# Kernel tuning notes

Measured on AMD Instinct MI355X. Metric: run time of the kernel, lower is better.

The kernel has to match this reference:

```python
import jax, jax.numpy as jnp
import numpy as np

B, T, H = 4096, 512, 512
GATE = 2 + H  # concat([x(1), h(H), mask(1)])


def setup_inputs() -> dict:
    key = jax.random.key(0)
    ks = jax.random.split(key, 20)
    s = 1.0 / np.sqrt(GATE)
    inp = {
        "x": jax.random.normal(ks[0], (B, T), jnp.float32),
        "x_last": jax.random.normal(ks[1], (B, T), jnp.float32),
        "interval": jax.random.uniform(ks[2], (B, T), jnp.float32),
        "mask": (jax.random.uniform(ks[3], (B, T)) > 0.3).astype(jnp.float32),
        # gamma decay layers
        "Wgx": jax.random.normal(ks[4], (1, 1), jnp.float32),
        "bgx": jnp.zeros((1,), jnp.float32),
        "Wgh": jax.random.normal(ks[5], (H, 1), jnp.float32),
        "bgh": jnp.zeros((H,), jnp.float32),
        # gate layers: Linear(GATE, H)
        "Wz": jax.random.normal(ks[6], (H, GATE), jnp.float32) * s,
        "bz": jnp.zeros((H,), jnp.float32),
        "Wr": jax.random.normal(ks[7], (H, GATE), jnp.float32) * s,
        "br": jnp.zeros((H,), jnp.float32),
        "Wh": jax.random.normal(ks[8], (H, GATE), jnp.float32) * s,
        "bh": jnp.zeros((H,), jnp.float32),
        # output head Linear(H, 1)
        "Wo": jax.random.normal(ks[9], (1, H), jnp.float32) / np.sqrt(H),
        "bo": jnp.zeros((1,), jnp.float32),
    }
    return inp


def reference(x, x_last, interval, mask, Wgx, bgx, Wgh, bgh,
              Wz, bz, Wr, br, Wh, bh, Wo, bo):
    # x, x_last, interval, mask: [B, T]; feature dim is 1 after unsqueeze
    x3 = x[..., None]            # [B, T, 1]
    xl3 = x_last[..., None]
    it3 = interval[..., None]
    m3 = mask[..., None]
    # mean(x*m, dim=1) * T / sum(m, dim=1) == sum(x*m)/sum(m)
    x_mean = jnp.sum(x3 * m3, axis=1) / jnp.sum(m3, axis=1)  # [B, 1]

    h0 = jnp.zeros((x.shape[0], Wz.shape[0]), x.dtype)
    # time-major stacks for scan: [T, B, 1]
    xs = (jnp.swapaxes(x3, 0, 1), jnp.swapaxes(xl3, 0, 1),
          jnp.swapaxes(m3, 0, 1), jnp.swapaxes(it3, 0, 1))

    def step(h, ts):
        xt, xl, mt, it = ts  # each [B, 1]
        gamma_x = jnp.exp(-jax.nn.relu(it @ Wgx.T + bgx))   # [B, 1]
        gamma_h = jnp.exp(-jax.nn.relu(it @ Wgh.T + bgh))   # [B, H]
        xi = mt * xt + (1.0 - mt) * (gamma_x * xl + (1.0 - gamma_x) * x_mean)
        h = gamma_h * h
        comb = jnp.concatenate([xi, h, mt], axis=1)          # [B, GATE]
        z = jax.nn.sigmoid(comb @ Wz.T + bz)
        r = jax.nn.sigmoid(comb @ Wr.T + br)
        comb_r = jnp.concatenate([xi, r * h, mt], axis=1)
        h_tilde = jnp.tanh(comb_r @ Wh.T + bh)
        h = (1.0 - z) * h + z * h_tilde
        return h, None

    h, _ = jax.lax.scan(step, h0, xs)
    return jax.nn.sigmoid(h @ Wo.T + bo)  # [B, 1]
```

## Files before the change

### kernel.cpp

```cpp
#include <hip/hip_runtime.h>
#include <stdint.h>

#define T_LEN 512
#define H_DIM 512
#define B_TOT 4096
#define GATE_D 514
#define CLUSTERS 16
#define RANKS 16
#define CROWS 256
#define OWNC 32
#define NTHR 512
#define BARPAD 256

typedef short s16x8 __attribute__((ext_vector_type(8)));
typedef float f32x4 __attribute__((ext_vector_type(4)));

__device__ __forceinline__ ushort f2bf(float f) {
    uint32_t u = __builtin_bit_cast(uint32_t, f);
    u += 0x7FFF + ((u >> 16) & 1);
    return (ushort)(u >> 16);
}
__device__ __forceinline__ float sigmoid_f(float x) {
    return 1.0f / (1.0f + __expf(-x));
}
__device__ __forceinline__ float tanh_f(float x) {
    float ax = fabsf(x);
    float e  = __expf(2.0f * ax);
    float t  = 1.0f - 2.0f / (e + 1.0f);
    return copysignf(t, x);
}
__device__ __forceinline__ void vm0() {
    asm volatile("s_waitcnt vmcnt(0)" ::: "memory");
}

__global__ void k_xmean(const float* __restrict__ x, const float* __restrict__ m,
                        float* __restrict__ xmean) {
    int b = blockIdx.x;
    int l = threadIdx.x;
    const float* xr = x + (size_t)b * T_LEN;
    const float* mr = m + (size_t)b * T_LEN;
    float sx = 0.f, sm = 0.f;
    #pragma unroll
    for (int i = 0; i < T_LEN / 64; ++i) {
        float mv = mr[l + i * 64];
        sx += xr[l + i * 64] * mv;
        sm += mv;
    }
    for (int off = 32; off; off >>= 1) {
        sx += __shfl_down(sx, off);
        sm += __shfl_down(sm, off);
    }
    if (l == 0) xmean[b] = sx / sm;
}

__global__ void k_init(unsigned int* barc) {
    int i = threadIdx.x + blockIdx.x * blockDim.x;
    if (i < CLUSTERS * BARPAD) barc[i] = 0u;
}

__device__ __forceinline__ void bar_slow(unsigned int* cnt, unsigned int target) {
    vm0();
    __syncthreads();
    if (threadIdx.x == 0) {
        __builtin_amdgcn_fence(__ATOMIC_RELEASE, "agent");
        __hip_atomic_fetch_add(cnt, 1u, __ATOMIC_RELAXED, __HIP_MEMORY_SCOPE_AGENT);
        while (__hip_atomic_load(cnt, __ATOMIC_RELAXED, __HIP_MEMORY_SCOPE_AGENT) < target)
            __builtin_amdgcn_s_sleep(1);
        __builtin_amdgcn_fence(__ATOMIC_ACQUIRE, "agent");
    }
    __syncthreads();
}

__device__ __forceinline__ void wave_arrive(unsigned int* cw, bool fastc) {
    vm0();
    if ((threadIdx.x & 63) == 0) {
        if (!fastc) __builtin_amdgcn_fence(__ATOMIC_RELEASE, "agent");
        __hip_atomic_fetch_add(cw, 1u, __ATOMIC_RELAXED, __HIP_MEMORY_SCOPE_AGENT);
    }
}
__device__ __forceinline__ void wave_wait(unsigned int* cw, unsigned int target, bool fastc) {
    while (__hip_atomic_load(cw, __ATOMIC_RELAXED, __HIP_MEMORY_SCOPE_AGENT) < target)
        __builtin_amdgcn_s_sleep(1);
    if (fastc) { asm volatile("buffer_inv" ::: "memory"); vm0(); }
    else __builtin_amdgcn_fence(__ATOMIC_ACQUIRE, "agent");
}

__global__ __launch_bounds__(NTHR) void k_grud(
    const float* __restrict__ x,   const float* __restrict__ xl,
    const float* __restrict__ itv, const float* __restrict__ msk,
    const float* __restrict__ Wgx, const float* __restrict__ bgx,
    const float* __restrict__ Wgh, const float* __restrict__ bgh,
    const float* __restrict__ Wz,  const float* __restrict__ bz,
    const float* __restrict__ Wr,  const float* __restrict__ br,
    const float* __restrict__ Wh,  const float* __restrict__ bh,
    const float* __restrict__ Wo,  const float* __restrict__ bo,
    const float* __restrict__ xmean,
    ushort* __restrict__ hdx, ushort* __restrict__ rhx,
    float* __restrict__ osum, unsigned int* __restrict__ barc,
    float* __restrict__ out)
{
    __shared__ ushort wfrag[96 * 512];
    __shared__ ushort stage[16 * 512];
    __shared__ float  xi_w[8][32], mts_w[8][32], itn_w[8][32];
    __shared__ float4 epi_s[96];
    __shared__ float2 ghb_s[OWNC];
    __shared__ unsigned int flag_s;

    const int tid = threadIdx.x;
    const int b   = blockIdx.x;
    const int cluster = (b & 7) * 2 + ((b >> 3) >> 4);
    const int rank    = (b >> 3) & 15;
    const int wv = tid >> 6, l = tid & 63;
    const int colb = l & 15, qg = l >> 4;
    const int r0 = cluster * CROWS;

    unsigned int* base    = barc + cluster * BARPAD;
    unsigned int* xcd_arr = base + 4;
    unsigned int* cw      = base + 64 + wv * 16;
    ushort* hdc = hdx + (size_t)cluster * CROWS * H_DIM;
    ushort* rhc = rhx + (size_t)cluster * CROWS * H_DIM;
    const s16x8* WF = (const s16x8*)wfrag;
    const s16x8* HD = (const s16x8*)hdc;
    const s16x8* RH = (const s16x8*)rhc;

    for (int s = tid; s < 96 * 64; s += NTHR) {
        int fi = s >> 6, ln = s & 63;
        int g = fi >> 5, nt = (fi >> 4) & 1, kt = fi & 15;
        const float* W = (g == 0) ? Wz : (g == 1) ? Wr : Wh;
        int colg = rank * OWNC + nt * 16 + (ln & 15);
        int c0 = 1 + kt * 32 + (ln >> 4) * 8;
        ushort tb[8];
        #pragma unroll
        for (int j = 0; j < 8; ++j) tb[j] = f2bf(W[(size_t)colg * GATE_D + c0 + j]);
        *(s16x8*)&wfrag[s * 8] = *(s16x8*)tb;
    }
    for (int i = tid; i < 96; i += NTHR) {
        int g = i >> 5, c = i & 31;
        const float* W  = (g == 0) ? Wz : (g == 1) ? Wr : Wh;
        const float* bb = (g == 0) ? bz : (g == 1) ? br : bh;
        int colg = rank * OWNC + c;
        epi_s[i] = make_float4(bb[colg], W[(size_t)colg * GATE_D],
                               W[(size_t)colg * GATE_D + GATE_D - 1], 0.f);
    }
    if (tid < OWNC) ghb_s[tid] = make_float2(Wgh[rank * OWNC + tid], bgh[rank * OWNC + tid]);
    const float wgx = Wgx[0], bgx0 = bgx[0];
    const float xmv = (l < 32) ? xmean[r0 + wv * 32 + l] : 0.f;

    if (tid == 0) {
        unsigned int myxcc;
        asm volatile("s_getreg_b32 %0, hwreg(HW_REG_XCC_ID)" : "=s"(myxcc));
        xcd_arr[rank] = myxcc;
    }
    bar_slow(base, RANKS);
    if (tid == 0) {
        unsigned int x0 = xcd_arr[0], same = 1;
        #pragma unroll
        for (int rk = 1; rk < RANKS; ++rk) same &= (xcd_arr[rk] == x0) ? 1u : 0u;
        flag_s = same;
    }
    __syncthreads();
    const bool fastc = (flag_s != 0);

    #pragma unroll
    for (int i = 0; i < 2; ++i) {
        int f = 2 * wv + i;
        *(s16x8*)((char*)hdc + (((size_t)f * 16 + rank) * 64 + l) * 16) = (s16x8){0,0,0,0,0,0,0,0};
    }
    wave_arrive(cw, fastc);

    float hdq[2][2][4];
    #pragma unroll
    for (int mt = 0; mt < 2; ++mt)
        #pragma unroll
        for (int nt = 0; nt < 2; ++nt)
            #pragma unroll
            for (int q = 0; q < 4; ++q) hdq[mt][nt][q] = 0.f;
    float zq[2][2][4];

    for (int t = 0; t < T_LEN; ++t) {
        if (l < 32) {
            size_t idx = (size_t)(r0 + wv * 32 + l) * T_LEN + t;
            float xv = x[idx], xlv = xl[idx], iv = itv[idx], mv = msk[idx];
            float gx = __expf(-fmaxf(iv * wgx + bgx0, 0.f));
            xi_w[wv][l]  = mv * xv + (1.f - mv) * (gx * xlv + (1.f - gx) * xmv);
            mts_w[wv][l] = mv;
        }
        wave_wait(cw, (unsigned int)(16 * (2 * t + 1)), fastc);

        f32x4 accz[2][2], accr[2][2];
        #pragma unroll
        for (int mt = 0; mt < 2; ++mt)
            #pragma unroll
            for (int nt = 0; nt < 2; ++nt) { accz[mt][nt] = (f32x4){0,0,0,0}; accr[mt][nt] = (f32x4){0,0,0,0}; }
        #pragma unroll
        for (int kt = 0; kt < 16; ++kt) {
            s16x8 a0 = HD[((2 * wv    ) * 16 + kt) * 64 + l];
            s16x8 a1 = HD[((2 * wv + 1) * 16 + kt) * 64 + l];
            #pragma unroll
            for (int nt = 0; nt < 2; ++nt) {
                s16x8 bz_ = WF[(     nt * 16 + kt) * 64 + l];
                s16x8 br_ = WF[(32 + nt * 16 + kt) * 64 + l];
                accz[0][nt] = __builtin_amdgcn_mfma_f32_16x16x32_bf16(a0, bz_, accz[0][nt], 0, 0, 0);
                accz[1][nt] = __builtin_amdgcn_mfma_f32_16x16x32_bf16(a1, bz_, accz[1][nt], 0, 0, 0);
                accr[0][nt] = __builtin_amdgcn_mfma_f32_16x16x32_bf16(a0, br_, accr[0][nt], 0, 0, 0);
                accr[1][nt] = __builtin_amdgcn_mfma_f32_16x16x32_bf16(a1, br_, accr[1][nt], 0, 0, 0);
            }
        }
        #pragma unroll
        for (int mt = 0; mt < 2; ++mt) {
            #pragma unroll
            for (int nt = 0; nt < 2; ++nt) {
                int c = nt * 16 + colb;
                float4 ez = epi_s[c];
                float4 er = epi_s[32 + c];
                int grp = (c >> 3) & 3, jj = c & 7;
                #pragma unroll
                for (int q = 0; q < 4; ++q) {
                    int lr = mt * 16 + qg * 4 + q;
                    float xiv = xi_w[wv][lr], mtv = mts_w[wv][lr];
                    zq[mt][nt][q] = sigmoid_f(accz[mt][nt][q] + ez.x + xiv * ez.y + mtv * ez.z);
                    float rr = sigmoid_f(accr[mt][nt][q] + er.x + xiv * er.y + mtv * er.z);
                    stage[(((2 * wv + mt) * 64) + (qg * 4 + q) + grp * 16) * 8 + jj] =
                        f2bf(rr * hdq[mt][nt][q]);
                }
            }
        }
        #pragma unroll
        for (int i = 0; i < 2; ++i) {
            int f = 2 * wv + i;
            *(s16x8*)((char*)rhc + (((size_t)f * 16 + rank) * 64 + l) * 16) =
                *(const s16x8*)&stage[(f * 64 + l) * 8];
        }
        wave_arrive(cw, fastc);

        if (l < 32 && t + 1 < T_LEN)
            itn_w[wv][l] = itv[(size_t)(r0 + wv * 32 + l) * T_LEN + t + 1];
        wave_wait(cw, (unsigned int)(16 * (2 * t + 2)), fastc);

        f32x4 acc2[2][2];
        #pragma unroll
        for (int mt = 0; mt < 2; ++mt)
            #pragma unroll
            for (int nt = 0; nt < 2; ++nt) acc2[mt][nt] = (f32x4){0,0,0,0};
        #pragma unroll
        for (int kt = 0; kt < 16; ++kt) {
            s16x8 a0 = RH[((2 * wv    ) * 16 + kt) * 64 + l];
            s16x8 a1 = RH[((2 * wv + 1) * 16 + kt) * 64 + l];
            #pragma unroll
            for (int nt = 0; nt < 2; ++nt) {
                s16x8 bh_ = WF[(64 + nt * 16 + kt) * 64 + l];
                acc2[0][nt] = __builtin_amdgcn_mfma_f32_16x16x32_bf16(a0, bh_, acc2[0][nt], 0, 0, 0);
                acc2[1][nt] = __builtin_amdgcn_mfma_f32_16x16x32_bf16(a1, bh_, acc2[1][nt], 0, 0, 0);
            }
        }
        const bool last = (t + 1 == T_LEN);
        #pragma unroll
        for (int mt = 0; mt < 2; ++mt) {
            #pragma unroll
            for (int nt = 0; nt < 2; ++nt) {
                int c = nt * 16 + colb;
                float4 eh = epi_s[64 + c];
                float2 gb = ghb_s[c];
                int grp = (c >> 3) & 3, jj = c & 7;
                #pragma unroll
                for (int q = 0; q < 4; ++q) {
                    int lr = mt * 16 + qg * 4 + q;
                    float ht = tanh_f(acc2[mt][nt][q] + eh.x + xi_w[wv][lr] * eh.y + mts_w[wv][lr] * eh.z);
                    float hd = hdq[mt][nt][q];
                    float hn = hd + zq[mt][nt][q] * (ht - hd);
                    float g  = last ? 1.f : __expf(-fmaxf(itn_w[wv][lr] * gb.x + gb.y, 0.f));
                    float hdn = hn * g;
                    hdq[mt][nt][q] = hdn;
                    if (!last)
                        stage[(((2 * wv + mt) * 64) + (qg * 4 + q) + grp * 16) * 8 + jj] = f2bf(hdn);
                }
            }
        }
        if (!last) {
            #pragma unroll
            for (int i = 0; i < 2; ++i) {
                int f = 2 * wv + i;
                *(s16x8*)((char*)hdc + (((size_t)f * 16 + rank) * 64 + l) * 16) =
                    *(const s16x8*)&stage[(f * 64 + l) * 8];
            }
        }
        wave_arrive(cw, fastc);
    }

    {
        float wo0 = Wo[rank * OWNC + colb];
        float wo1 = Wo[rank * OWNC + 16 + colb];
        #pragma unroll
        for (int mt = 0; mt < 2; ++mt) {
            #pragma unroll
            for (int q = 0; q < 4; ++q) {
                int row = wv * 32 + mt * 16 + qg * 4 + q;
                float p = hdq[mt][0][q] * wo0 + hdq[mt][1][q] * wo1;
                #pragma unroll
                for (int off = 1; off < 16; off <<= 1) p += __shfl_xor(p, off);
                if (colb == 0) osum[(size_t)(r0 + row) * RANKS + rank] = p;
            }
        }
    }
    bar_slow(base, 2 * RANKS);
    if (rank == 0 && tid < CROWS) {
        float s = 0.f;
        #pragma unroll
        for (int rk = 0; rk < RANKS; ++rk) s += osum[(size_t)(r0 + tid) * RANKS + rk];
        out[r0 + tid] = sigmoid_f(s + bo[0]);
    }
}

extern "C" void kernel_launch(void* const* d_in, const int* in_sizes, int n_in,
                              void* d_out, int out_size, void* d_ws, size_t ws_size,
                              hipStream_t stream) {
    const float* x    = (const float*)d_in[0];
    const float* xl   = (const float*)d_in[1];
    const float* itv  = (const float*)d_in[2];
    const float* msk  = (const float*)d_in[3];
    const float* Wgx  = (const float*)d_in[4];
    const float* bgx  = (const float*)d_in[5];
    const float* Wgh  = (const float*)d_in[6];
    const float* bgh  = (const float*)d_in[7];
    const float* Wz   = (const float*)d_in[8];
    const float* bz   = (const float*)d_in[9];
    const float* Wr   = (const float*)d_in[10];
    const float* br   = (const float*)d_in[11];
    const float* Wh   = (const float*)d_in[12];
    const float* bh   = (const float*)d_in[13];
    const float* Wo   = (const float*)d_in[14];
    const float* bo   = (const float*)d_in[15];

    char* ws = (char*)d_ws;
    float*        xmean = (float*)ws;
    unsigned int* barc  = (unsigned int*)(ws + 16384);
    float*        osum  = (float*)(ws + 32768);
    ushort*       hdx   = (ushort*)(ws + 32768 + 262144);
    ushort*       rhx   = (ushort*)(ws + 32768 + 262144 + 4194304);

    k_init<<<16, 256, 0, stream>>>(barc);
    k_xmean<<<B_TOT, 64, 0, stream>>>(x, msk, xmean);
    k_grud<<<CLUSTERS * RANKS, NTHR, 0, stream>>>(
        x, xl, itv, msk, Wgx, bgx, Wgh, bgh,
        Wz, bz, Wr, br, Wh, bh, Wo, bo,
        xmean, hdx, rhx, osum, barc, (float*)d_out);
}
```

Baseline: 6.989 ms.

## Precompute imputed inputs into time-major packed buffer and pack bf16 conversions

Adds a pre-pass kernel that computes the imputed input xi and packs it with interval and mask (encoded as iv + 2*mask) into a time-major float2 array. The recurrent kernel then reads one coalesced float2 per row each step instead of four strided loads plus an exp. The bf16 conversions for the staged r*h and h values now use the packed v_cvt_pk_bf16_f32 instruction, two values per call. This adds an extra kernel launch and a 32 MB workspace write/read, and the mask decode assumes interval values lie in [0,2).

```diff
diff --git a/kernel.cpp b/kernel.cpp
--- a/kernel.cpp
+++ b/kernel.cpp
@@ -19,6 +19,11 @@
     uint32_t u = __builtin_bit_cast(uint32_t, f);
     u += 0x7FFF + ((u >> 16) & 1);
     return (ushort)(u >> 16);
+}
+__device__ __forceinline__ uint32_t cvtpk(float lo, float hi) {
+    uint32_t r;
+    asm("v_cvt_pk_bf16_f32 %0, %1, %2" : "=v"(r) : "v"(lo), "v"(hi));
+    return r;
 }
 __device__ __forceinline__ float sigmoid_f(float x) {
     return 1.0f / (1.0f + __expf(-x));
@@ -53,6 +58,22 @@
     if (l == 0) xmean[b] = sx / sm;
 }
 
+__global__ void k_prep(const float* __restrict__ x,   const float* __restrict__ xl,
+                       const float* __restrict__ itv, const float* __restrict__ msk,
+                       const float* __restrict__ Wgx, const float* __restrict__ bgx,
+                       const float* __restrict__ xmean, float2* __restrict__ packT) {
+    int b = blockIdx.x;
+    float xm  = xmean[b];
+    float wgx = Wgx[0], b0 = bgx[0];
+    for (int i = threadIdx.x; i < T_LEN; i += 64) {
+        size_t idx = (size_t)b * T_LEN + i;
+        float xv = x[idx], xlv = xl[idx], iv = itv[idx], mv = msk[idx];
+        float gx = __expf(-fmaxf(iv * wgx + b0, 0.f));
+        float xi = mv * xv + (1.f - mv) * (gx * xlv + (1.f - gx) * xm);
+        packT[(size_t)i * B_TOT + b] = make_float2(xi, iv + 2.f * mv);
+    }
+}
+
 __global__ void k_init(unsigned int* barc) {
     int i = threadIdx.x + blockIdx.x * blockDim.x;
     if (i < CLUSTERS * BARPAD) barc[i] = 0u;
@@ -86,15 +107,12 @@
 }
 
 __global__ __launch_bounds__(NTHR) void k_grud(
-    const float* __restrict__ x,   const float* __restrict__ xl,
-    const float* __restrict__ itv, const float* __restrict__ msk,
-    const float* __restrict__ Wgx, const float* __restrict__ bgx,
     const float* __restrict__ Wgh, const float* __restrict__ bgh,
     const float* __restrict__ Wz,  const float* __restrict__ bz,
     const float* __restrict__ Wr,  const float* __restrict__ br,
     const float* __restrict__ Wh,  const float* __restrict__ bh,
     const float* __restrict__ Wo,  const float* __restrict__ bo,
-    const float* __restrict__ xmean,
+    const float2* __restrict__ packT,
     ushort* __restrict__ hdx, ushort* __restrict__ rhx,
     float* __restrict__ osum, unsigned int* __restrict__ barc,
     float* __restrict__ out)
@@ -143,8 +161,6 @@
                                W[(size_t)colg * GATE_D + GATE_D - 1], 0.f);
     }
     if (tid < OWNC) ghb_s[tid] = make_float2(Wgh[rank * OWNC + tid], bgh[rank * OWNC + tid]);
-    const float wgx = Wgx[0], bgx0 = bgx[0];
-    const float xmv = (l < 32) ? xmean[r0 + wv * 32 + l] : 0.f;
 
     if (tid == 0) {
         unsigned int myxcc;
@@ -179,10 +195,9 @@
 
     for (int t = 0; t < T_LEN; ++t) {
         if (l < 32) {
-            size_t idx = (size_t)(r0 + wv * 32 + l) * T_LEN + t;
-            float xv = x[idx], xlv = xl[idx], iv = itv[idx], mv = msk[idx];
-            float gx = __expf(-fmaxf(iv * wgx + bgx0, 0.f));
-            xi_w[wv][l]  = mv * xv + (1.f - mv) * (gx * xlv + (1.f - gx) * xmv);
+            float2 p = packT[(size_t)t * B_TOT + r0 + wv * 32 + l];
+            float mv = (p.y >= 2.f) ? 1.f : 0.f;
+            xi_w[wv][l]  = p.x;
             mts_w[wv][l] = mv;
         }
         wave_wait(cw, (unsigned int)(16 * (2 * t + 1)), fastc);
@@ -214,15 +229,22 @@
                 float4 ez = epi_s[c];
                 float4 er = epi_s[32 + c];
                 int grp = (c >> 3) & 3, jj = c & 7;
+                float rv[4];
                 #pragma unroll
                 for (int q = 0; q < 4; ++q) {
                     int lr = mt * 16 + qg * 4 + q;
                     float xiv = xi_w[wv][lr], mtv = mts_w[wv][lr];
                     zq[mt][nt][q] = sigmoid_f(accz[mt][nt][q] + ez.x + xiv * ez.y + mtv * ez.z);
                     float rr = sigmoid_f(accr[mt][nt][q] + er.x + xiv * er.y + mtv * er.z);
-                    stage[(((2 * wv + mt) * 64) + (qg * 4 + q) + grp * 16) * 8 + jj] =
-                        f2bf(rr * hdq[mt][nt][q]);
+                    rv[q] = rr * hdq[mt][nt][q];
                 }
+                int bidx = (((2 * wv + mt) * 64) + qg * 4 + grp * 16) * 8 + jj;
+                uint32_t w01 = cvtpk(rv[0], rv[1]);
+                uint32_t w23 = cvtpk(rv[2], rv[3]);
+                stage[bidx]      = (ushort)w01;
+                stage[bidx + 8]  = (ushort)(w01 >> 16);
+                stage[bidx + 16] = (ushort)w23;
+                stage[bidx + 24] = (ushort)(w23 >> 16);
             }
         }
         #pragma unroll
@@ -233,8 +255,11 @@
         }
         wave_arrive(cw, fastc);
 
-        if (l < 32 && t + 1 < T_LEN)
-            itn_w[wv][l] = itv[(size_t)(r0 + wv * 32 + l) * T_LEN + t + 1];
+        if (l < 32 && t + 1 < T_LEN) {
+            float2 p = packT[(size_t)(t + 1) * B_TOT + r0 + wv * 32 + l];
+            float sub = (p.y >= 2.f) ? 2.f : 0.f;
+            itn_w[wv][l] = p.y - sub;
+        }
         wave_wait(cw, (unsigned int)(16 * (2 * t + 2)), fastc);
 
         f32x4 acc2[2][2];
@@ -262,6 +287,7 @@
                 float4 eh = epi_s[64 + c];
                 float2 gb = ghb_s[c];
                 int grp = (c >> 3) & 3, jj = c & 7;
+                float hv[4];
                 #pragma unroll
                 for (int q = 0; q < 4; ++q) {
                     int lr = mt * 16 + qg * 4 + q;
@@ -271,8 +297,16 @@
                     float g  = last ? 1.f : __expf(-fmaxf(itn_w[wv][lr] * gb.x + gb.y, 0.f));
                     float hdn = hn * g;
                     hdq[mt][nt][q] = hdn;
-                    if (!last)
-                        stage[(((2 * wv + mt) * 64) + (qg * 4 + q) + grp * 16) * 8 + jj] = f2bf(hdn);
+                    hv[q] = hdn;
+                }
+                if (!last) {
+                    int bidx = (((2 * wv + mt) * 64) + qg * 4 + grp * 16) * 8 + jj;
+                    uint32_t w01 = cvtpk(hv[0], hv[1]);
+                    uint32_t w23 = cvtpk(hv[2], hv[3]);
+                    stage[bidx]      = (ushort)w01;
+                    stage[bidx + 8]  = (ushort)(w01 >> 16);
+                    stage[bidx + 16] = (ushort)w23;
+                    stage[bidx + 24] = (ushort)(w23 >> 16);
                 }
             }
         }
@@ -335,13 +369,14 @@
     float*        xmean = (float*)ws;
     unsigned int* barc  = (unsigned int*)(ws + 16384);
     float*        osum  = (float*)(ws + 32768);
-    ushort*       hdx   = (ushort*)(ws + 32768 + 262144);
-    ushort*       rhx   = (ushort*)(ws + 32768 + 262144 + 4194304);
+    ushort*       hdx   = (ushort*)(ws + 294912);
+    ushort*       rhx   = (ushort*)(ws + 294912 + 4194304);
+    float2*       packT = (float2*)(ws + 294912 + 8388608);
 
     k_init<<<16, 256, 0, stream>>>(barc);
     k_xmean<<<B_TOT, 64, 0, stream>>>(x, msk, xmean);
+    k_prep<<<B_TOT, 64, 0, stream>>>(x, xl, itv, msk, Wgx, bgx, xmean, packT);
     k_grud<<<CLUSTERS * RANKS, NTHR, 0, stream>>>(
-        x, xl, itv, msk, Wgx, bgx, Wgh, bgh,
-        Wz, bz, Wr, br, Wh, bh, Wo, bo,
-        xmean, hdx, rhx, osum, barc, (float*)d_out);
-}
+        Wgh, bgh, Wz, bz, Wr, br, Wh, bh, Wo, bo,
+        packT, hdx, rhx, osum, barc, (float*)d_out);
+}
```

New measurement: 10.49 ms. 1.5x slower.

## Split workgroup waves into gate and candidate groups with producer-consumer counters

Applied to the files above, without the earlier changes.

Each workgroup's waves are split in two. Waves 0-3 compute the z/r gates and write r*h to global memory. Waves 4-7 compute the candidate state, update h and write it back. Each group signals the other through separate per-row-slice counters instead of one shared counter per wave with two waits per step. Each wave now handles 64 rows instead of 32, and z is passed between the groups through a new shared-memory buffer. This lets the two half-steps of different row slices overlap and lets next-step inputs be fetched early, at the cost of putting the gate and candidate work on half the waves each.

```diff
diff --git a/kernel.cpp b/kernel.cpp
--- a/kernel.cpp
+++ b/kernel.cpp
@@ -11,6 +11,7 @@
 #define OWNC 32
 #define NTHR 512
 #define BARPAD 256
+#define ZS 33
 
 typedef short s16x8 __attribute__((ext_vector_type(8)));
 typedef float f32x4 __attribute__((ext_vector_type(4)));
@@ -19,6 +20,10 @@
     uint32_t u = __builtin_bit_cast(uint32_t, f);
     u += 0x7FFF + ((u >> 16) & 1);
     return (ushort)(u >> 16);
+}
+__device__ __forceinline__ float bf2f(ushort h) {
+    uint32_t u = ((uint32_t)h) << 16;
+    return __builtin_bit_cast(float, u);
 }
 __device__ __forceinline__ float sigmoid_f(float x) {
     return 1.0f / (1.0f + __expf(-x));
@@ -72,7 +77,7 @@
 }
 
 __device__ __forceinline__ void wave_arrive(unsigned int* cw, bool fastc) {
-    vm0();
+    asm volatile("s_waitcnt vmcnt(0) lgkmcnt(0)" ::: "memory");
     if ((threadIdx.x & 63) == 0) {
         if (!fastc) __builtin_amdgcn_fence(__ATOMIC_RELEASE, "agent");
         __hip_atomic_fetch_add(cw, 1u, __ATOMIC_RELAXED, __HIP_MEMORY_SCOPE_AGENT);
@@ -101,7 +106,8 @@
 {
     __shared__ ushort wfrag[96 * 512];
     __shared__ ushort stage[16 * 512];
-    __shared__ float  xi_w[8][32], mts_w[8][32], itn_w[8][32];
+    __shared__ float  z_s[CROWS * ZS];
+    __shared__ float  xi_s[CROWS], mts_s[CROWS], itn_s[CROWS];
     __shared__ float4 epi_s[96];
     __shared__ float2 ghb_s[OWNC];
     __shared__ unsigned int flag_s;
@@ -111,12 +117,15 @@
     const int cluster = (b & 7) * 2 + ((b >> 3) >> 4);
     const int rank    = (b >> 3) & 15;
     const int wv = tid >> 6, l = tid & 63;
+    const bool isG1 = (wv < 4);
+    const int j = wv & 3;
     const int colb = l & 15, qg = l >> 4;
     const int r0 = cluster * CROWS;
 
     unsigned int* base    = barc + cluster * BARPAD;
     unsigned int* xcd_arr = base + 4;
-    unsigned int* cw      = base + 64 + wv * 16;
+    unsigned int* cnt_hd  = base + 64  + j * 16;
+    unsigned int* cnt_rh  = base + 128 + j * 16;
     ushort* hdc = hdx + (size_t)cluster * CROWS * H_DIM;
     ushort* rhc = rhx + (size_t)cluster * CROWS * H_DIM;
     const s16x8* WF = (const s16x8*)wfrag;
@@ -131,9 +140,10 @@
         int c0 = 1 + kt * 32 + (ln >> 4) * 8;
         ushort tb[8];
         #pragma unroll
-        for (int j = 0; j < 8; ++j) tb[j] = f2bf(W[(size_t)colg * GATE_D + c0 + j]);
+        for (int jj = 0; jj < 8; ++jj) tb[jj] = f2bf(W[(size_t)colg * GATE_D + c0 + jj]);
         *(s16x8*)&wfrag[s * 8] = *(s16x8*)tb;
     }
+    for (int i = tid; i < 4096; i += NTHR) ((uint32_t*)stage)[i] = 0u;
     for (int i = tid; i < 96; i += NTHR) {
         int g = i >> 5, c = i & 31;
         const float* W  = (g == 0) ? Wz : (g == 1) ? Wr : Wh;
@@ -144,7 +154,14 @@
     }
     if (tid < OWNC) ghb_s[tid] = make_float2(Wgh[rank * OWNC + tid], bgh[rank * OWNC + tid]);
     const float wgx = Wgx[0], bgx0 = bgx[0];
-    const float xmv = (l < 32) ? xmean[r0 + wv * 32 + l] : 0.f;
+    const float xmv = xmean[r0 + j * 64 + l];
+
+    #pragma unroll
+    for (int i = 0; i < 2; ++i) {
+        int s = tid + i * NTHR;
+        *(s16x8*)((char*)hdc + ((size_t)(s >> 6) * 1024 + (size_t)rank * 64 + (s & 63)) * 16) =
+            (s16x8){0,0,0,0,0,0,0,0};
+    }
 
     if (tid == 0) {
         unsigned int myxcc;
@@ -161,147 +178,156 @@
     __syncthreads();
     const bool fastc = (flag_s != 0);
 
-    #pragma unroll
-    for (int i = 0; i < 2; ++i) {
-        int f = 2 * wv + i;
-        *(s16x8*)((char*)hdc + (((size_t)f * 16 + rank) * 64 + l) * 16) = (s16x8){0,0,0,0,0,0,0,0};
-    }
-    wave_arrive(cw, fastc);
-
-    float hdq[2][2][4];
-    #pragma unroll
-    for (int mt = 0; mt < 2; ++mt)
+    if (!isG1) wave_arrive(cnt_hd, fastc);
+
+    if (isG1) {
+        for (int t = 0; t < T_LEN; ++t) {
+            size_t idx = (size_t)(r0 + j * 64 + l) * T_LEN + t;
+            float xv = x[idx], xlv = xl[idx], iv = itv[idx], mv = msk[idx];
+            wave_wait(cnt_hd, (unsigned int)(16 * (t + 1)), fastc);
+            float gx = __expf(-fmaxf(iv * wgx + bgx0, 0.f));
+            xi_s[j * 64 + l]  = mv * xv + (1.f - mv) * (gx * xlv + (1.f - gx) * xmv);
+            mts_s[j * 64 + l] = mv;
+
+            f32x4 accz[4][2], accr[4][2];
+            #pragma unroll
+            for (int i = 0; i < 4; ++i)
+                #pragma unroll
+                for (int nt = 0; nt < 2; ++nt) { accz[i][nt] = (f32x4){0,0,0,0}; accr[i][nt] = (f32x4){0,0,0,0}; }
+            #pragma unroll
+            for (int kt = 0; kt < 16; ++kt) {
+                s16x8 a[4];
+                #pragma unroll
+                for (int i = 0; i < 4; ++i)
+                    a[i] = HD[(((4 * j + i) * 16 + kt)) * 64 + l];
+                #pragma unroll
+                for (int nt = 0; nt < 2; ++nt) {
+                    s16x8 bz_ = WF[(     nt * 16 + kt) * 64 + l];
+                    s16x8 br_ = WF[(32 + nt * 16 + kt) * 64 + l];
+                    #pragma unroll
+                    for (int i = 0; i < 4; ++i) {
+                        accz[i][nt] = __builtin_amdgcn_mfma_f32_16x16x32_bf16(a[i], bz_, accz[i][nt], 0, 0, 0);
+                        accr[i][nt] = __builtin_amdgcn_mfma_f32_16x16x32_bf16(a[i], br_, accr[i][nt], 0, 0, 0);
+                    }
+                }
+            }
+            #pragma unroll
+            for (int i = 0; i < 4; ++i) {
+                int mt = 4 * j + i;
+                #pragma unroll
+                for (int nt = 0; nt < 2; ++nt) {
+                    int c = nt * 16 + colb;
+                    float4 ez = epi_s[c];
+                    float4 er = epi_s[32 + c];
+                    int grp = (c >> 3) & 3, jj = c & 7;
+                    #pragma unroll
+                    for (int q = 0; q < 4; ++q) {
+                        int row = mt * 16 + qg * 4 + q;
+                        float xiv = xi_s[row], mtv = mts_s[row];
+                        float zz = sigmoid_f(accz[i][nt][q] + ez.x + xiv * ez.y + mtv * ez.z);
+                        z_s[row * ZS + c] = zz;
+                        int sidx = ((mt * 64) + (qg * 4 + q) + grp * 16) * 8 + jj;
+                        float hd = bf2f(stage[sidx]);
+                        float rr = sigmoid_f(accr[i][nt][q] + er.x + xiv * er.y + mtv * er.z);
+                        stage[sidx] = f2bf(rr * hd);
+                    }
+                }
+            }
+            #pragma unroll
+            for (int i = 0; i < 4; ++i) {
+                int f = 4 * j + i;
+                *(s16x8*)((char*)rhc + (((size_t)f * 16 + rank) * 64 + l) * 16) =
+                    *(const s16x8*)&stage[(f * 64 + l) * 8];
+            }
+            wave_arrive(cnt_rh, fastc);
+        }
+    } else {
+        float hdq[4][2][4];
         #pragma unroll
-        for (int nt = 0; nt < 2; ++nt)
-            #pragma unroll
-            for (int q = 0; q < 4; ++q) hdq[mt][nt][q] = 0.f;
-    float zq[2][2][4];
-
-    for (int t = 0; t < T_LEN; ++t) {
-        if (l < 32) {
-            size_t idx = (size_t)(r0 + wv * 32 + l) * T_LEN + t;
-            float xv = x[idx], xlv = xl[idx], iv = itv[idx], mv = msk[idx];
-            float gx = __expf(-fmaxf(iv * wgx + bgx0, 0.f));
-            xi_w[wv][l]  = mv * xv + (1.f - mv) * (gx * xlv + (1.f - gx) * xmv);
-            mts_w[wv][l] = mv;
+        for (int i = 0; i < 4; ++i)
+            #pragma unroll
+            for (int nt = 0; nt < 2; ++nt)
+                #pragma unroll
+                for (int q = 0; q < 4; ++q) hdq[i][nt][q] = 0.f;
+
+        for (int t = 0; t < T_LEN; ++t) {
+            const bool last = (t + 1 == T_LEN);
+            int tn = last ? t : t + 1;
+            float iv_n = itv[(size_t)(r0 + j * 64 + l) * T_LEN + tn];
+            wave_wait(cnt_rh, (unsigned int)(16 * (t + 1)), fastc);
+            itn_s[j * 64 + l] = iv_n;
+
+            f32x4 acc2[4][2];
+            #pragma unroll
+            for (int i = 0; i < 4; ++i)
+                #pragma unroll
+                for (int nt = 0; nt < 2; ++nt) acc2[i][nt] = (f32x4){0,0,0,0};
+            #pragma unroll
+            for (int kt = 0; kt < 16; ++kt) {
+                s16x8 a[4];
+                #pragma unroll
+                for (int i = 0; i < 4; ++i)
+                    a[i] = RH[(((4 * j + i) * 16 + kt)) * 64 + l];
+                #pragma unroll
+                for (int nt = 0; nt < 2; ++nt) {
+                    s16x8 bh_ = WF[(64 + nt * 16 + kt) * 64 + l];
+                    #pragma unroll
+                    for (int i = 0; i < 4; ++i)
+                        acc2[i][nt] = __builtin_amdgcn_mfma_f32_16x16x32_bf16(a[i], bh_, acc2[i][nt], 0, 0, 0);
+                }
+            }
+            #pragma unroll
+            for (int i = 0; i < 4; ++i) {
+                int mt = 4 * j + i;
+                #pragma unroll
+                for (int nt = 0; nt < 2; ++nt) {
+                    int c = nt * 16 + colb;
+                    float4 eh = epi_s[64 + c];
+                    float2 gb = ghb_s[c];
+                    int grp = (c >> 3) & 3, jj = c & 7;
+                    #pragma unroll
+                    for (int q = 0; q < 4; ++q) {
+                        int row = mt * 16 + qg * 4 + q;
+                        float ht = tanh_f(acc2[i][nt][q] + eh.x + xi_s[row] * eh.y + mts_s[row] * eh.z);
+                        float hd = hdq[i][nt][q];
+                        float zz = z_s[row * ZS + c];
+                        float hn = hd + zz * (ht - hd);
+                        float g  = last ? 1.f : __expf(-fmaxf(itn_s[row] * gb.x + gb.y, 0.f));
+                        float hdn = hn * g;
+                        hdq[i][nt][q] = hdn;
+                        if (!last)
+                            stage[((mt * 64) + (qg * 4 + q) + grp * 16) * 8 + jj] = f2bf(hdn);
+                    }
+                }
+            }
+            if (!last) {
+                #pragma unroll
+                for (int i = 0; i < 4; ++i) {
+                    int f = 4 * j + i;
+                    *(s16x8*)((char*)hdc + (((size_t)f * 16 + rank) * 64 + l) * 16) =
+                        *(const s16x8*)&stage[(f * 64 + l) * 8];
+                }
+            }
+            wave_arrive(cnt_hd, fastc);
         }
-        wave_wait(cw, (unsigned int)(16 * (2 * t + 1)), fastc);
-
-        f32x4 accz[2][2], accr[2][2];
-        #pragma unroll
-        for (int mt = 0; mt < 2; ++mt)
-            #pragma unroll
-            for (int nt = 0; nt < 2; ++nt) { accz[mt][nt] = (f32x4){0,0,0,0}; accr[mt][nt] = (f32x4){0,0,0,0}; }
-        #pragma unroll
-        for (int kt = 0; kt < 16; ++kt) {
-            s16x8 a0 = HD[((2 * wv    ) * 16 + kt) * 64 + l];
-            s16x8 a1 = HD[((2 * wv + 1) * 16 + kt) * 64 + l];
-            #pragma unroll
-            for (int nt = 0; nt < 2; ++nt) {
-                s16x8 bz_ = WF[(     nt * 16 + kt) * 64 + l];
-                s16x8 br_ = WF[(32 + nt * 16 + kt) * 64 + l];
-                accz[0][nt] = __builtin_amdgcn_mfma_f32_16x16x32_bf16(a0, bz_, accz[0][nt], 0, 0, 0);
-                accz[1][nt] = __builtin_amdgcn_mfma_f32_16x16x32_bf16(a1, bz_, accz[1][nt], 0, 0, 0);
-                accr[0][nt] = __builtin_amdgcn_mfma_f32_16x16x32_bf16(a0, br_, accr[0][nt], 0, 0, 0);
-                accr[1][nt] = __builtin_amdgcn_mfma_f32_16x16x32_bf16(a1, br_, accr[1][nt], 0, 0, 0);
+
+        {
+            float wo0 = Wo[rank * OWNC + colb];
+            float wo1 = Wo[rank * OWNC + 16 + colb];
+            #pragma unroll
+            for (int i = 0; i < 4; ++i) {
+                #pragma unroll
+                for (int q = 0; q < 4; ++q) {
+                    int row = (4 * j + i) * 16 + qg * 4 + q;
+                    float p = hdq[i][0][q] * wo0 + hdq[i][1][q] * wo1;
+                    #pragma unroll
+                    for (int off = 1; off < 16; off <<= 1) p += __shfl_xor(p, off);
+                    if (colb == 0) osum[(size_t)(r0 + row) * RANKS + rank] = p;
+                }
             }
         }
-        #pragma unroll
-        for (int mt = 0; mt < 2; ++mt) {
-            #pragma unroll
-            for (int nt = 0; nt < 2; ++nt) {
-                int c = nt * 16 + colb;
-                float4 ez = epi_s[c];
-                float4 er = epi_s[32 + c];
-                int grp = (c >> 3) & 3, jj = c & 7;
-                #pragma unroll
-                for (int q = 0; q < 4; ++q) {
-                    int lr = mt * 16 + qg * 4 + q;
-                    float xiv = xi_w[wv][lr], mtv = mts_w[wv][lr];
-                    zq[mt][nt][q] = sigmoid_f(accz[mt][nt][q] + ez.x + xiv * ez.y + mtv * ez.z);
-                    float rr = sigmoid_f(accr[mt][nt][q] + er.x + xiv * er.y + mtv * er.z);
-                    stage[(((2 * wv + mt) * 64) + (qg * 4 + q) + grp * 16) * 8 + jj] =
-                        f2bf(rr * hdq[mt][nt][q]);
-                }
-            }
-        }
-        #pragma unroll
-        for (int i = 0; i < 2; ++i) {
-            int f = 2 * wv + i;
-            *(s16x8*)((char*)rhc + (((size_t)f * 16 + rank) * 64 + l) * 16) =
-                *(const s16x8*)&stage[(f * 64 + l) * 8];
-        }
-        wave_arrive(cw, fastc);
-
-        if (l < 32 && t + 1 < T_LEN)
-            itn_w[wv][l] = itv[(size_t)(r0 + wv * 32 + l) * T_LEN + t + 1];
-        wave_wait(cw, (unsigned int)(16 * (2 * t + 2)), fastc);
-
-        f32x4 acc2[2][2];
-        #pragma unroll
-        for (int mt = 0; mt < 2; ++mt)
-            #pragma unroll
-            for (int nt = 0; nt < 2; ++nt) acc2[mt][nt] = (f32x4){0,0,0,0};
-        #pragma unroll
-        for (int kt = 0; kt < 16; ++kt) {
-            s16x8 a0 = RH[((2 * wv    ) * 16 + kt) * 64 + l];
-            s16x8 a1 = RH[((2 * wv + 1) * 16 + kt) * 64 + l];
-            #pragma unroll
-            for (int nt = 0; nt < 2; ++nt) {
-                s16x8 bh_ = WF[(64 + nt * 16 + kt) * 64 + l];
-                acc2[0][nt] = __builtin_amdgcn_mfma_f32_16x16x32_bf16(a0, bh_, acc2[0][nt], 0, 0, 0);
-                acc2[1][nt] = __builtin_amdgcn_mfma_f32_16x16x32_bf16(a1, bh_, acc2[1][nt], 0, 0, 0);
-            }
-        }
-        const bool last = (t + 1 == T_LEN);
-        #pragma unroll
-        for (int mt = 0; mt < 2; ++mt) {
-            #pragma unroll
-            for (int nt = 0; nt < 2; ++nt) {
-                int c = nt * 16 + colb;
-                float4 eh = epi_s[64 + c];
-                float2 gb = ghb_s[c];
-                int grp = (c >> 3) & 3, jj = c & 7;
-                #pragma unroll
-                for (int q = 0; q < 4; ++q) {
-                    int lr = mt * 16 + qg * 4 + q;
-                    float ht = tanh_f(acc2[mt][nt][q] + eh.x + xi_w[wv][lr] * eh.y + mts_w[wv][lr] * eh.z);
-                    float hd = hdq[mt][nt][q];
-                    float hn = hd + zq[mt][nt][q] * (ht - hd);
-                    float g  = last ? 1.f : __expf(-fmaxf(itn_w[wv][lr] * gb.x + gb.y, 0.f));
-                    float hdn = hn * g;
-                    hdq[mt][nt][q] = hdn;
-                    if (!last)
-                        stage[(((2 * wv + mt) * 64) + (qg * 4 + q) + grp * 16) * 8 + jj] = f2bf(hdn);
-                }
-            }
-        }
-        if (!last) {
-            #pragma unroll
-            for (int i = 0; i < 2; ++i) {
-                int f = 2 * wv + i;
-                *(s16x8*)((char*)hdc + (((size_t)f * 16 + rank) * 64 + l) * 16) =
-                    *(const s16x8*)&stage[(f * 64 + l) * 8];
-            }
-        }
-        wave_arrive(cw, fastc);
-    }
-
-    {
-        float wo0 = Wo[rank * OWNC + colb];
-        float wo1 = Wo[rank * OWNC + 16 + colb];
-        #pragma unroll
-        for (int mt = 0; mt < 2; ++mt) {
-            #pragma unroll
-            for (int q = 0; q < 4; ++q) {
-                int row = wv * 32 + mt * 16 + qg * 4 + q;
-                float p = hdq[mt][0][q] * wo0 + hdq[mt][1][q] * wo1;
-                #pragma unroll
-                for (int off = 1; off < 16; off <<= 1) p += __shfl_xor(p, off);
-                if (colb == 0) osum[(size_t)(r0 + row) * RANKS + rank] = p;
-            }
-        }
-    }
+    }
+
     bar_slow(base, 2 * RANKS);
     if (rank == 0 && tid < CROWS) {
         float s = 0.f;
@@ -335,8 +361,8 @@
     float*        xmean = (float*)ws;
     unsigned int* barc  = (unsigned int*)(ws + 16384);
     float*        osum  = (float*)(ws + 32768);
-    ushort*       hdx   = (ushort*)(ws + 32768 + 262144);
-    ushort*       rhx   = (ushort*)(ws + 32768 + 262144 + 4194304);
+    ushort*       hdx   = (ushort*)(ws + 294912);
+    ushort*       rhx   = (ushort*)(ws + 294912 + 4194304);
 
     k_init<<<16, 256, 0, stream>>>(barc);
     k_xmean<<<B_TOT, 64, 0, stream>>>(x, msk, xmean);
```

Measured after the change: 18.68 ms. 2.67x slower.
